# Kernel tuning notes

Hardware: AMD Instinct MI355X
Metric: run time of the kernel (lower is better)

The kernel has to match this reference:

```python
import jax, jax.numpy as jnp
import numpy as np


def setup_inputs() -> dict:
    key = jax.random.key(0)
    k1, k2, k3 = jax.random.split(key, 3)
    B, C, T = 2048, 32000, 16384
    preds = jax.random.normal(k1, (B, C), dtype=jnp.float32)
    flat_targets = jax.random.randint(k2, (T,), 0, C, dtype=jnp.int64)
    row_ids = jnp.sort(jax.random.randint(k3, (T,), 0, B, dtype=jnp.int64))
    return {"preds": preds, "flat_targets": flat_targets, "row_ids": row_ids}


def reference(preds, flat_targets, row_ids):
    # Original: softmax(preds) then per-sample gather -> log -> sum, then
    # sum over batch / batch_size. softmax+log fused as log_softmax; the
    # ragged per-sample sums collapse into a single global sum since the
    # loss is sum over all gathered targets divided by batch_size.
    logp = jax.nn.log_softmax(preds, axis=1)          # [B, C]
    nll = -logp[row_ids, flat_targets]                # [T] ragged gather
    batch_size = preds.shape[0]
    return nll.sum() / batch_size
```

## Files before the change

kernel.cpp:

```cpp
#include <hip/hip_runtime.h>
#include <hip/hip_bf16.h>
#include <math.h>

__global__ __launch_bounds__(256) void row_lse_gather_kernel(
    const float* __restrict__ preds, const int* __restrict__ tgt,
    const int* __restrict__ rows, float* __restrict__ partial,
    int C, int T) {
    const int row = blockIdx.x;
    const size_t base = (size_t)row * C;
    const float4* __restrict__ p =
        reinterpret_cast<const float4*>(preds + base);
    const int n4 = C >> 2;

    float s0 = 0.f, s1 = 0.f, s2 = 0.f, s3 = 0.f;
    for (int i = threadIdx.x; i < n4; i += 256) {
        float4 v = p[i];
        s0 += __expf(v.x);
        s1 += __expf(v.y);
        s2 += __expf(v.z);
        s3 += __expf(v.w);
    }
    float s = (s0 + s1) + (s2 + s3);
    #pragma unroll
    for (int off = 32; off > 0; off >>= 1) s += __shfl_xor(s, off);

    __shared__ float ss[4];
    const int wave = threadIdx.x >> 6;
    const int lane = threadIdx.x & 63;
    if (lane == 0) ss[wave] = s;
    __syncthreads();

    if (wave == 0) {
        float S = ss[0] + ss[1] + ss[2] + ss[3];
        float lse = __logf(S);

        int lo, hi;
        {
            int l = 0, r = T;
            while (l < r) { int m = (l + r) >> 1; if (rows[m] < row) l = m + 1; else r = m; }
            lo = l;
        }
        {
            int l = lo, r = T;
            while (l < r) { int m = (l + r) >> 1; if (rows[m] <= row) l = m + 1; else r = m; }
            hi = l;
        }
        const int cnt = hi - lo;

        float g = 0.f;
        for (int i = lo + lane; i < hi; i += 64)
            g += preds[base + tgt[i]];
        #pragma unroll
        for (int off = 32; off > 0; off >>= 1) g += __shfl_xor(g, off);

        if (lane == 0) partial[row] = (float)cnt * lse - g;
    }
}

__global__ __launch_bounds__(256) void finalize_kernel(
    const float* __restrict__ partial, float* __restrict__ out,
    int B, float invB) {
    float a = 0.f;
    for (int i = threadIdx.x; i < B; i += 256) a += partial[i];
    #pragma unroll
    for (int off = 32; off > 0; off >>= 1) a += __shfl_xor(a, off);

    __shared__ float ws[4];
    const int wave = threadIdx.x >> 6;
    if ((threadIdx.x & 63) == 0) ws[wave] = a;
    __syncthreads();
    if (threadIdx.x == 0)
        out[0] = (ws[0] + ws[1] + ws[2] + ws[3]) * invB;
}

extern "C" void kernel_launch(void* const* d_in, const int* in_sizes, int n_in,
                              void* d_out, int out_size, void* d_ws, size_t ws_size,
                              hipStream_t stream) {
    const float* preds = (const float*)d_in[0];
    const int*   tgt   = (const int*)d_in[1];
    const int*   rows  = (const int*)d_in[2];
    float* out = (float*)d_out;

    const int T = in_sizes[1];
    const int C = 32000;
    const int B = in_sizes[0] / C;

    float* partial = (float*)d_ws;

    row_lse_gather_kernel<<<B, 256, 0, stream>>>(preds, tgt, rows, partial, C, T);
    finalize_kernel<<<1, 256, 0, stream>>>(partial, out, B, 1.0f / (float)B);
}
```

Before: 49.67 us.

## Prefetch row loads in registers and move target gather to a finalize kernel

```diff
diff --git a/kernel.cpp b/kernel.cpp
--- a/kernel.cpp
+++ b/kernel.cpp
@@ -2,75 +2,85 @@
 #include <hip/hip_bf16.h>
 #include <math.h>
 
-__global__ __launch_bounds__(256) void row_lse_gather_kernel(
-    const float* __restrict__ preds, const int* __restrict__ tgt,
-    const int* __restrict__ rows, float* __restrict__ partial,
-    int C, int T) {
+constexpr int kC    = 32000;
+constexpr int kN4   = kC / 4;
+constexpr int kNT   = 256;
+constexpr int kFull = kN4 / kNT;
+
+__global__ __launch_bounds__(kNT) void row_lse_kernel(
+    const float* __restrict__ preds, float* __restrict__ lse) {
     const int row = blockIdx.x;
-    const size_t base = (size_t)row * C;
-    const float4* __restrict__ p =
-        reinterpret_cast<const float4*>(preds + base);
-    const int n4 = C >> 2;
+    const size_t base = (size_t)row * kC;
+    const float4* __restrict__ p = reinterpret_cast<const float4*>(preds + base);
+    const int t    = threadIdx.x;
+    const int lane = t & 63;
+    const int wave = t >> 6;
 
     float s0 = 0.f, s1 = 0.f, s2 = 0.f, s3 = 0.f;
-    for (int i = threadIdx.x; i < n4; i += 256) {
-        float4 v = p[i];
+
+    float4 tail;
+    if (wave == 0) tail = p[kFull * kNT + lane];
+
+    float4 buf0 = p[t];
+    float4 buf1 = p[t + kNT];
+    float4 buf2 = p[t + 2 * kNT];
+    float4 buf3 = p[t + 3 * kNT];
+
+    #pragma unroll
+    for (int k = 0; k < kFull; ++k) {
+        float4 v;
+        switch (k & 3) {
+            case 0: v = buf0; if (k + 4 < kFull) buf0 = p[t + (k + 4) * kNT]; break;
+            case 1: v = buf1; if (k + 4 < kFull) buf1 = p[t + (k + 4) * kNT]; break;
+            case 2: v = buf2; if (k + 4 < kFull) buf2 = p[t + (k + 4) * kNT]; break;
+            default: v = buf3; if (k + 4 < kFull) buf3 = p[t + (k + 4) * kNT]; break;
+        }
         s0 += __expf(v.x);
         s1 += __expf(v.y);
         s2 += __expf(v.z);
         s3 += __expf(v.w);
     }
+    if (wave == 0) {
+        s0 += __expf(tail.x);
+        s1 += __expf(tail.y);
+        s2 += __expf(tail.z);
+        s3 += __expf(tail.w);
+    }
+
     float s = (s0 + s1) + (s2 + s3);
     #pragma unroll
     for (int off = 32; off > 0; off >>= 1) s += __shfl_xor(s, off);
 
     __shared__ float ss[4];
-    const int wave = threadIdx.x >> 6;
-    const int lane = threadIdx.x & 63;
     if (lane == 0) ss[wave] = s;
     __syncthreads();
-
-    if (wave == 0) {
-        float S = ss[0] + ss[1] + ss[2] + ss[3];
-        float lse = __logf(S);
-
-        int lo, hi;
-        {
-            int l = 0, r = T;
-            while (l < r) { int m = (l + r) >> 1; if (rows[m] < row) l = m + 1; else r = m; }
-            lo = l;
-        }
-        {
-            int l = lo, r = T;
-            while (l < r) { int m = (l + r) >> 1; if (rows[m] <= row) l = m + 1; else r = m; }
-            hi = l;
-        }
-        const int cnt = hi - lo;
-
-        float g = 0.f;
-        for (int i = lo + lane; i < hi; i += 64)
-            g += preds[base + tgt[i]];
-        #pragma unroll
-        for (int off = 32; off > 0; off >>= 1) g += __shfl_xor(g, off);
-
-        if (lane == 0) partial[row] = (float)cnt * lse - g;
-    }
+    if (t == 0) lse[row] = __logf(ss[0] + ss[1] + ss[2] + ss[3]);
 }
 
-__global__ __launch_bounds__(256) void finalize_kernel(
-    const float* __restrict__ partial, float* __restrict__ out,
-    int B, float invB) {
-    float a = 0.f;
-    for (int i = threadIdx.x; i < B; i += 256) a += partial[i];
+__global__ __launch_bounds__(1024) void gather_finalize_kernel(
+    const float* __restrict__ preds, const float* __restrict__ lse,
+    const int* __restrict__ tgt, const int* __restrict__ rows,
+    float* __restrict__ out, int T, float invB) {
+    float acc = 0.f;
+    for (int i = threadIdx.x; i < T; i += 1024) {
+        int r = rows[i];
+        int c = tgt[i];
+        acc += lse[r] - preds[(size_t)r * kC + c];
+    }
     #pragma unroll
-    for (int off = 32; off > 0; off >>= 1) a += __shfl_xor(a, off);
+    for (int off = 32; off > 0; off >>= 1) acc += __shfl_xor(acc, off);
 
-    __shared__ float ws[4];
+    __shared__ float ws[16];
+    const int lane = threadIdx.x & 63;
     const int wave = threadIdx.x >> 6;
-    if ((threadIdx.x & 63) == 0) ws[wave] = a;
+    if (lane == 0) ws[wave] = acc;
     __syncthreads();
-    if (threadIdx.x == 0)
-        out[0] = (ws[0] + ws[1] + ws[2] + ws[3]) * invB;
+    if (threadIdx.x == 0) {
+        float a = 0.f;
+        #pragma unroll
+        for (int w = 0; w < 16; ++w) a += ws[w];
+        out[0] = a * invB;
+    }
 }
 
 extern "C" void kernel_launch(void* const* d_in, const int* in_sizes, int n_in,
@@ -82,11 +92,11 @@
     float* out = (float*)d_out;
 
     const int T = in_sizes[1];
-    const int C = 32000;
-    const int B = in_sizes[0] / C;
+    const int B = in_sizes[0] / kC;
 
-    float* partial = (float*)d_ws;
+    float* lse = (float*)d_ws;
 
-    row_lse_gather_kernel<<<B, 256, 0, stream>>>(preds, tgt, rows, partial, C, T);
-    finalize_kernel<<<1, 256, 0, stream>>>(partial, out, B, 1.0f / (float)B);
+    row_lse_kernel<<<B, kNT, 0, stream>>>(preds, lse);
+    gather_finalize_kernel<<<1, 1024, 0, stream>>>(preds, lse, tgt, rows, out,
+                                                   T, 1.0f / (float)B);
 }
```

Measured after the change: 67.47 us. +35.9%, slower.
